# Optimization experiments

Measured on AMD Instinct MI355X. Metric: run time of the kernel, lower is better.

## Reference

```python
import jax, jax.numpy as jnp
import numpy as np

N_TOKEN = 267735
D_EMBED = 1024
D_PROJ = 1024
DIV_VAL = 4
CUTOFFS = [20000, 40000, 200000, N_TOKEN]   # cutoffs + [n_token]
ENDS = [0] + CUTOFFS                         # cutoff_ends
N_CLUSTERS = len(CUTOFFS) - 1                # 3
HEAD_SIZE = CUTOFFS[0] + N_CLUSTERS          # 20003
N = 1024                                     # len*bsz


def setup_inputs() -> dict:
    key = jax.random.key(0)
    ks = jax.random.split(key, 16)
    d_embs = [D_EMBED // DIV_VAL ** i for i in range(4)]  # 1024,256,64,16
    sizes = [HEAD_SIZE] + [ENDS[i + 1] - ENDS[i] for i in range(1, 4)]  # 20003,20000,160000,67735
    s = 0.02
    inp = {
        'hidden': jax.random.normal(ks[0], (N, D_PROJ), dtype=jnp.float32),
        'target': jax.random.randint(ks[1], (N,), 0, N_TOKEN, dtype=jnp.int32),
    }
    for i in range(4):
        inp[f'w{i}'] = jax.random.normal(ks[2 + 3 * i], (sizes[i], d_embs[i]), dtype=jnp.float32) * s
        inp[f'b{i}'] = jnp.zeros((sizes[i],), dtype=jnp.float32)
        inp[f'p{i}'] = jax.random.normal(ks[3 + 3 * i], (D_PROJ, d_embs[i]), dtype=jnp.float32) * s
    return inp


def _logit(h, w, b, p):
    # F.linear(hidden, proj.t()) -> h @ p ; F.linear(., weight, bias) -> @ w.T + b
    return (h @ p) @ w.T + b


def reference(hidden, target, w0, b0, p0, w1, b1, p1, w2, b2, p2, w3, b3, p3):
    head_lp = jax.nn.log_softmax(_logit(hidden, w0, b0, p0), axis=1)  # [N, HEAD_SIZE]
    tails = [(w1, b1, p1), (w2, b2, p2), (w3, b3, p3)]
    lps = []
    # shortlist cluster: gather target logprob directly from head
    t0 = jnp.clip(target, 0, CUTOFFS[0] - 1)
    lps.append(jnp.take_along_axis(head_lp, t0[:, None], axis=1)[:, 0])
    # tail clusters: small projected matmul + log_softmax + gather, combined with cluster logprob head_lp[:, -i]
    for i in range(1, 4):
        l, r = ENDS[i], ENDS[i + 1]
        ti = jnp.clip(target - l, 0, r - l - 1)
        tail_lp = jax.nn.log_softmax(_logit(hidden, *tails[i - 1]), axis=1)  # [N, r-l]
        lps.append(head_lp[:, -i] + jnp.take_along_axis(tail_lp, ti[:, None], axis=1)[:, 0])
    masks = [(target >= ENDS[i]) & (target < ENDS[i + 1]) for i in range(4)]
    logprob = jnp.select(masks, lps)
    return -logprob  # [N] per-token NLL, original order (keep_order=True)
```

## Files before the change

kernel.cpp:

```cpp
#include <hip/hip_runtime.h>
#include <hip/hip_bf16.h>
#include <math.h>

#define NTOK 1024
#define DPROJ 1024
#define PSTRIDE 1376
#define HEADS 20003
#define LOG2E 1.4426950408889634f
#define LN2   0.6931471805599453f
#define WSCALE (4.0f * LOG2E)
#define PSCALE 0.25f

#if __has_builtin(__builtin_amdgcn_exp2f)
#define EXP2(x) __builtin_amdgcn_exp2f(x)
#else
#define EXP2(x) exp2f(x)
#endif

#define MFMA8(a, b, c) __builtin_amdgcn_mfma_f32_16x16x32_fp8_fp8(a, b, c, 0, 0, 0)

typedef __attribute__((ext_vector_type(8))) short bf16x8;
typedef __attribute__((ext_vector_type(4))) float f32x4;
typedef long long i64;

__device__ __forceinline__ short f2bf(float f) {
    unsigned u = __float_as_uint(f);
    u += 0x7fffu + ((u >> 16) & 1u);
    return (short)(u >> 16);
}
__device__ __forceinline__ unsigned pk4fp8(float a, float b, float c, float d) {
    unsigned v = __builtin_amdgcn_cvt_pk_fp8_f32(a, b, 0, false);
    v = __builtin_amdgcn_cvt_pk_fp8_f32(c, d, v, true);
    return v;
}
__device__ __forceinline__ unsigned char fp8_1(float a) {
    return (unsigned char)(__builtin_amdgcn_cvt_pk_fp8_f32(a, a, 0, false) & 0xff);
}
__device__ __forceinline__ i64 wfrag(const float* wp) {
    float4 x = *(const float4*)(wp);
    float4 y = *(const float4*)(wp + 4);
    unsigned lo = pk4fp8(x.x * WSCALE, x.y * WSCALE, x.z * WSCALE, x.w * WSCALE);
    unsigned hi = pk4fp8(y.x * WSCALE, y.y * WSCALE, y.z * WSCALE, y.w * WSCALE);
    return (i64)(((unsigned long long)hi << 32) | lo);
}

#define NB0 157
#define NB1 79
#define NB2 625
#define NB3 265
#define NBTOT (NB0 + NB1 + NB2 + NB3)

#define EB0N 20096
#define EB1N 20224
#define EB2N 160000
#define EB3N 67840
#define EBTOT (EB0N + EB1N + EB2N + EB3N)

__global__ __launch_bounds__(256) void prep(const float* __restrict__ hidden,
                                            const float* __restrict__ p0,
                                            const float* __restrict__ p1,
                                            const float* __restrict__ p2,
                                            const float* __restrict__ p3,
                                            const float* __restrict__ b0,
                                            const float* __restrict__ b1,
                                            const float* __restrict__ b2,
                                            const float* __restrict__ b3,
                                            short* __restrict__ hbP,
                                            short* __restrict__ pTbP0,
                                            short* __restrict__ pTbP1,
                                            short* __restrict__ pTbP2,
                                            short* __restrict__ pTbP3,
                                            float* __restrict__ sums,
                                            unsigned char* __restrict__ pk3,
                                            float* __restrict__ eb0,
                                            float* __restrict__ eb1,
                                            float* __restrict__ eb2,
                                            float* __restrict__ eb3) {
    __shared__ float tile[64][65];
    int bid = blockIdx.x, tid = threadIdx.x;
    if (bid >= 418) {
        int g = (bid - 418) * 256 + tid;
        if (g < EB0N) {
            eb0[g] = (g < HEADS) ? exp2f(b0[g] * LOG2E) : 0.f;
        } else if (g < EB0N + EB1N) {
            int i = g - EB0N;
            eb1[i] = (i < 20000) ? exp2f(b1[i] * LOG2E) : 0.f;
        } else if (g < EB0N + EB1N + EB2N) {
            int i = g - EB0N - EB1N;
            eb2[i] = exp2f(b2[i] * LOG2E);
        } else if (g < EBTOT) {
            int i = g - EB0N - EB1N - EB2N;
            eb3[i] = (i < 67735) ? exp2f(b3[i] * LOG2E) : 0.f;
        }
        return;
    }
    if (bid == 416) {
        float4 z = {0.f, 0.f, 0.f, 0.f};
        #pragma unroll
        for (int i = 0; i < 4; ++i) *((float4*)sums + i * 256 + tid) = z;
        return;
    }
    if (bid == 417) {
        int4 z = {0, 0, 0, 0};
        #pragma unroll
        for (int i = 0; i < 8; ++i) *((int4*)pk3 + i * 256 + tid) = z;
        return;
    }
    if (bid < 64) {
        int tt = bid;
        #pragma unroll
        for (int q = 0; q < 8; ++q) {
            int fi = q * 256 + tid;
            int l = fi & 63;
            int row = tt * 16 + (l & 15);
            int kb = (fi >> 6) * 32 + (l >> 4) * 8;
            const float* hp = hidden + row * 1024 + kb;
            float4 x = *(const float4*)hp;
            float4 y = *(const float4*)(hp + 4);
            bf16x8 o;
            o[0]=f2bf(x.x); o[1]=f2bf(x.y); o[2]=f2bf(x.z); o[3]=f2bf(x.w);
            o[4]=f2bf(y.x); o[5]=f2bf(y.y); o[6]=f2bf(y.z); o[7]=f2bf(y.w);
            *(bf16x8*)(hbP + (size_t)tt * 16384 + fi * 8) = o;
        }
        return;
    }
    int lb = bid - 64;
    const float* p; short* dst; int d, kt, jb;
    if (lb < 256)      { p = p0; dst = pTbP0; d = 1024; kt = lb >> 4; jb = lb & 15; }
    else if (lb < 320) { lb -= 256; p = p1; dst = pTbP1; d = 256; kt = lb >> 2; jb = lb & 3; }
    else if (lb < 336) { lb -= 320; p = p2; dst = pTbP2; d = 64;  kt = lb; jb = 0; }
    else               { lb -= 336; p = p3; dst = pTbP3; d = 16;  kt = lb; jb = 0; }
    int k0 = kt * 64, j0 = jb * 64;
    int tx = tid & 63, ty = tid >> 6;
    #pragma unroll
    for (int rr = 0; rr < 16; ++rr) {
        int k = k0 + ty * 16 + rr;
        int j = j0 + tx;
        if (j < d) tile[ty * 16 + rr][tx] = p[k * d + j];
    }
    __syncthreads();
    int ch = tid >> 5;
    int jtl = ch >> 1, ksl = ch & 1;
    int jt = jb * 4 + jtl;
    if (jt * 16 < d) {
        #pragma unroll
        for (int li = 0; li < 2; ++li) {
            int l = (tid & 31) + li * 32;
            int jl = jtl * 16 + (l & 15);
            int kl = ksl * 32 + (l >> 4) * 8;
            bf16x8 o;
            #pragma unroll
            for (int e = 0; e < 8; ++e) o[e] = f2bf(tile[kl + e][jl]);
            *(bf16x8*)(dst + ((size_t)jt * 32 + kt * 2 + ksl) * 512 + l * 8) = o;
        }
    }
}

__global__ __launch_bounds__(256) void proj(const short* __restrict__ hbP,
                                            const short* __restrict__ pTbP0,
                                            const short* __restrict__ pTbP1,
                                            const short* __restrict__ pTbP2,
                                            const short* __restrict__ pTbP3,
                                            float* __restrict__ projf,
                                            unsigned char* __restrict__ pk0,
                                            unsigned char* __restrict__ pk1,
                                            unsigned char* __restrict__ pk2,
                                            unsigned char* __restrict__ pk3) {
    __shared__ float spackf[16][72];
    __shared__ unsigned char sp8[1024];
    int tt = blockIdx.x, jbG = blockIdx.y, tid = threadIdx.x;
    const short* pB; unsigned char* pkc; int d, KSp, coloff, jb;
    if (jbG < 16)      { pB = pTbP0; pkc = pk0; d = 1024; KSp = 32; coloff = 0;    jb = jbG; }
    else if (jbG < 20) { pB = pTbP1; pkc = pk1; d = 256;  KSp = 8;  coloff = 1024; jb = jbG - 16; }
    else if (jbG == 20){ pB = pTbP2; pkc = pk2; d = 64;   KSp = 2;  coloff = 1280; jb = 0; }
    else               { pB = pTbP3; pkc = pk3; d = 16;   KSp = 1;  coloff = 1344; jb = 0; }
    int w = tid >> 6, lane = tid & 63;
    int l16 = lane & 15, quad = lane >> 4;
    int jt = jb * 4 + w;
    if (jt * 16 < d) {
        const short* ap = hbP + ((size_t)tt * 32) * 512 + lane * 8;
        const short* bp = pB  + ((size_t)jt * 32) * 512 + lane * 8;
        f32x4 x0 = {0,0,0,0}, x1 = {0,0,0,0};
        #pragma unroll
        for (int ks = 0; ks < 16; ++ks) {
            bf16x8 a0 = *(const bf16x8*)(ap + ks * 512);
            bf16x8 b0 = *(const bf16x8*)(bp + ks * 512);
            bf16x8 a1 = *(const bf16x8*)(ap + (ks + 16) * 512);
            bf16x8 b1 = *(const bf16x8*)(bp + (ks + 16) * 512);
            x0 = __builtin_amdgcn_mfma_f32_16x16x32_bf16(a0, b0, x0, 0, 0, 0);
            x1 = __builtin_amdgcn_mfma_f32_16x16x32_bf16(a1, b1, x1, 0, 0, 0);
        }
        f32x4 acc = x0 + x1;
        int kk = w * 16 + l16;
        #pragma unroll
        for (int r = 0; r < 4; ++r) {
            int tok = quad * 4 + r;
            spackf[tok][kk] = acc[r];
            sp8[(kk >> 5) * 512 + ((kk & 31) >> 3) * 128 + tok * 8 + (kk & 7)] = fp8_1(acc[r] * PSCALE);
        }
    }
    __syncthreads();
    int j0g = jb * 64;
    int dcols = min(64, d - j0g);
    {
        int row = tid >> 4, cb = (tid & 15) * 4;
        if (cb < dcols) {
            float4 v = *(const float4*)&spackf[row][cb];
            *(float4*)&projf[(tt * 16 + row) * PSTRIDE + coloff + j0g + cb] = v;
        }
    }
    {
        int nbytes = 16 * dcols;
        if (tid * 4 < nbytes) {
            unsigned char* gdst = pkc + ((size_t)tt * KSp + (j0g >> 5)) * 512;
            *(unsigned*)(gdst + tid * 4) = *(const unsigned*)(sp8 + tid * 4);
        }
    }
}

__device__ __forceinline__ void stage16k(const unsigned char* g, unsigned char* l,
                                         int wave, int lane) {
    const unsigned char* gs = g + wave * 4096 + lane * 16;
    unsigned char* ls = l + wave * 4096;
    #pragma unroll
    for (int i = 0; i < 4; ++i)
        __builtin_amdgcn_global_load_lds(
            (const __attribute__((address_space(1))) unsigned*)(gs + i * 1024),
            (__attribute__((address_space(3))) unsigned*)(ls + i * 1024), 16, 0, 0);
}

__device__ __forceinline__ void lse_head(const float* __restrict__ w,
                                         const float* __restrict__ eb,
                                         const unsigned char* __restrict__ pk,
                                         float* __restrict__ part, int bid,
                                         unsigned char (*sbuf)[16384], float* bsum) {
    int tid = threadIdx.x;
    int wave = tid >> 6, lane = tid & 63;
    int quad = lane >> 4, l16 = lane & 15;
    int v0 = bid * 128 + wave * 32;

    for (int i = tid; i < NTOK; i += 256) bsum[i] = 0.f;

    i64 areg[2][32];
    float ee[2][4];
    #pragma unroll
    for (int vt = 0; vt < 2; ++vt) {
        int va = v0 + vt * 16 + l16;
        #pragma unroll
        for (int ks = 0; ks < 32; ++ks) {
            areg[vt][ks] = (va < HEADS) ? wfrag(w + (long)va * 1024 + ks * 32 + quad * 8) : 0;
        }
        #pragma unroll
        for (int r = 0; r < 4; ++r)
            ee[vt][r] = eb[v0 + vt * 16 + quad * 4 + r];
    }

    stage16k(pk, sbuf[0], wave, lane);
    __syncthreads();
    for (int tt = 0; tt < 64; ++tt) {
        if (tt < 63) stage16k(pk + (size_t)(tt + 1) * 16384, sbuf[(tt + 1) & 1], wave, lane);
        const unsigned char* sb = sbuf[tt & 1];
        f32x4 x0 = {0,0,0,0}, x1 = x0, x2 = x0, x3 = x0;
        __builtin_amdgcn_s_setprio(1);
        #pragma unroll
        for (int j = 0; j < 16; ++j) {
            i64 b0 = *(const i64*)(sb + j * 512 + lane * 8);
            i64 b1 = *(const i64*)(sb + (j + 16) * 512 + lane * 8);
            x0 = MFMA8(areg[0][j],      b0, x0);
            x1 = MFMA8(areg[0][j + 16], b1, x1);
            x2 = MFMA8(areg[1][j],      b0, x2);
            x3 = MFMA8(areg[1][j + 16], b1, x3);
        }
        __builtin_amdgcn_s_setprio(0);
        f32x4 a0 = x0 + x1, a1 = x2 + x3;
        float e0 = EXP2(a0[0]) * ee[0][0], e1 = EXP2(a0[1]) * ee[0][1];
        e0 += EXP2(a0[2]) * ee[0][2];  e1 += EXP2(a0[3]) * ee[0][3];
        e0 += EXP2(a1[0]) * ee[1][0];  e1 += EXP2(a1[1]) * ee[1][1];
        e0 += EXP2(a1[2]) * ee[1][2];  e1 += EXP2(a1[3]) * ee[1][3];
        float e = e0 + e1;
        e += __shfl_xor(e, 16, 64);
        e += __shfl_xor(e, 32, 64);
        if (lane < 16) atomicAdd(&bsum[tt * 16 + lane], e);
        __syncthreads();
    }
    *((float4*)part + tid) = *((const float4*)bsum + tid);
}

template <int KS, int VT>
__device__ __forceinline__ void lse_tail(const float* __restrict__ w,
                                         const float* __restrict__ eb,
                                         const unsigned char* __restrict__ pk,
                                         float* __restrict__ part,
                                         int V, int D, int bid, float* bsum) {
    int tid = threadIdx.x;
    int wave = tid >> 6, lane = tid & 63;
    int quad = lane >> 4, l16 = lane & 15;
    int v0 = bid * (64 * VT) + wave * (16 * VT);

    for (int i = tid; i < NTOK; i += 256) bsum[i] = 0.f;
    __syncthreads();

    i64 areg[VT][KS];
    float ee[VT][4];
    #pragma unroll
    for (int vt = 0; vt < VT; ++vt) {
        int va = v0 + vt * 16 + l16;
        #pragma unroll
        for (int ks = 0; ks < KS; ++ks) {
            int k = ks * 32 + quad * 8;
            areg[vt][ks] = (va < V && k < D) ? wfrag(w + (long)va * D + k) : 0;
        }
        #pragma unroll
        for (int r = 0; r < 4; ++r)
            ee[vt][r] = eb[v0 + vt * 16 + quad * 4 + r];
    }

    const i64* base = (const i64*)pk;
    i64 bn[KS];
    #pragma unroll
    for (int k = 0; k < KS; ++k) bn[k] = base[k * 64 + lane];
    for (int tt = 0; tt < 64; ++tt) {
        i64 bc[KS];
        #pragma unroll
        for (int k = 0; k < KS; ++k) bc[k] = bn[k];
        if (tt < 63) {
            const i64* nb = base + (size_t)(tt + 1) * KS * 64;
            #pragma unroll
            for (int k = 0; k < KS; ++k) bn[k] = nb[k * 64 + lane];
        }
        f32x4 accs[VT];
        __builtin_amdgcn_s_setprio(1);
        #pragma unroll
        for (int vt = 0; vt < VT; ++vt) {
            if constexpr (KS >= 4) {
                f32x4 y0 = {0,0,0,0}, y1 = {0,0,0,0};
                #pragma unroll
                for (int j = 0; j < KS / 2; ++j) {
                    y0 = MFMA8(areg[vt][j],          bc[j],          y0);
                    y1 = MFMA8(areg[vt][KS/2 + j],   bc[KS/2 + j],   y1);
                }
                accs[vt] = y0 + y1;
            } else if constexpr (KS == 2) {
                f32x4 y = {0,0,0,0};
                y = MFMA8(areg[vt][0], bc[0], y);
                y = MFMA8(areg[vt][1], bc[1], y);
                accs[vt] = y;
            } else {
                f32x4 y = {0,0,0,0};
                accs[vt] = MFMA8(areg[vt][0], bc[0], y);
            }
        }
        __builtin_amdgcn_s_setprio(0);
        float e0 = 0.f, e1 = 0.f;
        #pragma unroll
        for (int vt = 0; vt < VT; ++vt) {
            e0 += EXP2(accs[vt][0]) * ee[vt][0];
            e1 += EXP2(accs[vt][1]) * ee[vt][1];
            e0 += EXP2(accs[vt][2]) * ee[vt][2];
            e1 += EXP2(accs[vt][3]) * ee[vt][3];
        }
        float e = e0 + e1;
        e += __shfl_xor(e, 16, 64);
        e += __shfl_xor(e, 32, 64);
        if (lane < 16) atomicAdd(&bsum[tt * 16 + lane], e);
    }
    __syncthreads();
    *((float4*)part + tid) = *((const float4*)bsum + tid);
}

__global__ __launch_bounds__(256, 2) void lse_all(const float* __restrict__ w0, const float* __restrict__ eb0,
                                                  const float* __restrict__ w1, const float* __restrict__ eb1,
                                                  const float* __restrict__ w2, const float* __restrict__ eb2,
                                                  const float* __restrict__ w3, const float* __restrict__ eb3,
                                                  const unsigned char* __restrict__ pk0,
                                                  const unsigned char* __restrict__ pk1,
                                                  const unsigned char* __restrict__ pk2,
                                                  const unsigned char* __restrict__ pk3,
                                                  float* __restrict__ part) {
    __shared__ unsigned char sbuf[2][16384];
    __shared__ float bsum[NTOK];
    int bid = blockIdx.x;
    float* slab = part + (size_t)bid * NTOK;
    if (bid < NB0) {
        lse_head(w0, eb0, pk0, slab, bid, sbuf, bsum);
    } else if (bid < NB0 + NB1) {
        lse_tail<8, 4>(w1, eb1, pk1, slab, 20000,  256, bid - NB0, bsum);
    } else if (bid < NB0 + NB1 + NB2) {
        lse_tail<2, 4>(w2, eb2, pk2, slab, 160000, 64,  bid - NB0 - NB1, bsum);
    } else {
        lse_tail<1, 4>(w3, eb3, pk3, slab, 67735,  16,  bid - NB0 - NB1 - NB2, bsum);
    }
}

__global__ __launch_bounds__(256) void reduce_part(const float* __restrict__ part,
                                                   float* __restrict__ sums) {
    int bid = blockIdx.x;
    int c = bid >> 5, rem = bid & 31, q = rem >> 3, sl = rem & 7;
    const int off[4] = {0, NB0, NB0 + NB1, NB0 + NB1 + NB2};
    const int cnt[4] = {NB0, NB1, NB2, NB3};
    int tok = q * 256 + threadIdx.x;
    const float* p = part + (size_t)off[c] * NTOK + tok;
    int n = cnt[c];
    float s0 = 0.f, s1 = 0.f, s2 = 0.f, s3 = 0.f;
    int b = sl;
    for (; b + 24 < n; b += 32) {
        s0 += p[(size_t)b * NTOK];
        s1 += p[(size_t)(b + 8) * NTOK];
        s2 += p[(size_t)(b + 16) * NTOK];
        s3 += p[(size_t)(b + 24) * NTOK];
    }
    for (; b < n; b += 8) s0 += p[(size_t)b * NTOK];
    float s = (s0 + s1) + (s2 + s3);
    atomicAdd(&sums[c * NTOK + tok], s);
}

__global__ __launch_bounds__(256) void finalize(const int* __restrict__ target,
                                                const float* __restrict__ projf,
                                                const float* __restrict__ sums,
                                                const float* __restrict__ w0, const float* __restrict__ b0,
                                                const float* __restrict__ w1, const float* __restrict__ b1,
                                                const float* __restrict__ w2, const float* __restrict__ b2,
                                                const float* __restrict__ w3, const float* __restrict__ b3,
                                                float* __restrict__ out) {
    int wave = threadIdx.x >> 6, lane = threadIdx.x & 63;
    int row = blockIdx.x * 4 + wave;
    int t = target[row];
    int c = (t < 20000) ? 0 : (t < 40000) ? 1 : (t < 200000) ? 2 : 3;
    int col0 = (c == 0) ? t : (HEADS - c);
    const float* pr = projf + row * PSTRIDE;

    float s = 0.f;
    for (int k = lane; k < DPROJ; k += 64) s += pr[k] * w0[col0 * DPROJ + k];
    #pragma unroll
    for (int off = 32; off; off >>= 1) s += __shfl_xor(s, off, 64);
    float hl = s + b0[col0];
    float lse0 = __log2f(sums[row]) * LN2;

    float res;
    if (c == 0) {
        res = lse0 - hl;
    } else {
        const float* wc; const float* bc; int d, coloff, l;
        if (c == 1)      { wc = w1; bc = b1; d = 256; coloff = 1024; l = 20000; }
        else if (c == 2) { wc = w2; bc = b2; d = 64;  coloff = 1280; l = 40000; }
        else             { wc = w3; bc = b3; d = 16;  coloff = 1344; l = 200000; }
        int tc = t - l;
        float s2 = 0.f;
        for (int k = lane; k < d; k += 64) s2 += pr[coloff + k] * wc[tc * d + k];
        #pragma unroll
        for (int off = 32; off; off >>= 1) s2 += __shfl_xor(s2, off, 64);
        float tl = s2 + bc[tc];
        float lsec = __log2f(sums[c * NTOK + row]) * LN2;
        res = lse0 - hl + lsec - tl;
    }
    if (lane == 0) out[row] = res;
}


extern "C" void kernel_launch(void* const* d_in, const int* in_sizes, int n_in,
                              void* d_out, int out_size, void* d_ws, size_t ws_size,
                              hipStream_t stream) {
    const float* hidden = (const float*)d_in[0];
    const int*   target = (const int*)d_in[1];
    const float* w0 = (const float*)d_in[2];
    const float* b0 = (const float*)d_in[3];
    const float* p0 = (const float*)d_in[4];
    const float* w1 = (const float*)d_in[5];
    const float* b1 = (const float*)d_in[6];
    const float* p1 = (const float*)d_in[7];
    const float* w2 = (const float*)d_in[8];
    const float* b2 = (const float*)d_in[9];
    const float* p2 = (const float*)d_in[10];
    const float* w3 = (const float*)d_in[11];
    const float* b3 = (const float*)d_in[12];
    const float* p3 = (const float*)d_in[13];

    short* base = (short*)d_ws;
    short* hbP   = base;
    short* pTbP0 = base + 1048576;
    short* pTbP1 = base + 2097152;
    short* pTbP2 = base + 2359296;
    short* pTbP3 = base + 2424832;
    float* projf = (float*)((char*)d_ws + 4882432);
    unsigned char* pk0 = (unsigned char*)d_ws + 10518528;
    unsigned char* pk1 = pk0 + 1048576;
    unsigned char* pk2 = pk1 + 262144;
    unsigned char* pk3 = pk2 + 65536;
    float* sums  = (float*)((char*)d_ws + 11927552);
    float* part  = (float*)((char*)d_ws + 11943936);
    float* eb0   = (float*)((char*)d_ws + 16556032);
    float* eb1   = (float*)((char*)d_ws + 16636416);
    float* eb2   = (float*)((char*)d_ws + 16717312);
    float* eb3   = (float*)((char*)d_ws + 17357312);

    prep<<<1466, 256, 0, stream>>>(hidden, p0, p1, p2, p3, b0, b1, b2, b3,
                                   hbP, pTbP0, pTbP1, pTbP2, pTbP3, sums, pk3,
                                   eb0, eb1, eb2, eb3);
    proj<<<dim3(64, 22), 256, 0, stream>>>(hbP, pTbP0, pTbP1, pTbP2, pTbP3,
                                           projf, pk0, pk1, pk2, pk3);
    lse_all<<<NBTOT, 256, 0, stream>>>(w0, eb0, w1, eb1, w2, eb2, w3, eb3,
                                       pk0, pk1, pk2, pk3, part);
    reduce_part<<<128, 256, 0, stream>>>(part, sums);
    finalize<<<256, 256, 0, stream>>>(target, projf, sums,
                                      w0, b0, w1, b1, w2, b2, w3, b3, (float*)d_out);
}
```

Measured before the change: 323.6 us.

## Split head and tail LSE into separate kernels with token-halved head blocks

Splits the fused lse_all kernel into a head kernel and a tails kernel. The head kernel now uses twice as many blocks, each covering half the tokens, so the 157-block head work spreads across more CUs, and each half-block writes into its half of a shared slab. The tail kernel drops the 32KB LDS staging buffer, raises launch bounds to 4 blocks per CU and changes the vocab-tile template parameters (fewer blocks for clusters 2 and 3). Exp-bias padding and the workspace offsets are adjusted to match. The trade-off is that each head block now reloads its full weight fragments for only half the token work, which doubles the head weight reads. It also adds a launch, and the two kernels on the same stream run back to back rather than overlapping.

```diff
diff --git a/kernel.cpp b/kernel.cpp
--- a/kernel.cpp
+++ b/kernel.cpp
@@ -45,15 +45,17 @@
 }
 
 #define NB0 157
-#define NB1 79
-#define NB2 625
-#define NB3 265
-#define NBTOT (NB0 + NB1 + NB2 + NB3)
+#define NB0G 314
+#define NB1T 157
+#define NB2T 313
+#define NB3T 133
+#define NBT (NB1T + NB2T + NB3T)
+#define NSLAB (NB0 + NBT)
 
 #define EB0N 20096
-#define EB1N 20224
-#define EB2N 160000
-#define EB3N 67840
+#define EB1N 20096
+#define EB2N 160256
+#define EB3N 68096
 #define EBTOT (EB0N + EB1N + EB2N + EB3N)
 
 __global__ __launch_bounds__(256) void prep(const float* __restrict__ hidden,
@@ -87,7 +89,7 @@
             eb1[i] = (i < 20000) ? exp2f(b1[i] * LOG2E) : 0.f;
         } else if (g < EB0N + EB1N + EB2N) {
             int i = g - EB0N - EB1N;
-            eb2[i] = exp2f(b2[i] * LOG2E);
+            eb2[i] = (i < 160000) ? exp2f(b2[i] * LOG2E) : 0.f;
         } else if (g < EBTOT) {
             int i = g - EB0N - EB1N - EB2N;
             eb3[i] = (i < 67735) ? exp2f(b3[i] * LOG2E) : 0.f;
@@ -229,17 +231,20 @@
             (__attribute__((address_space(3))) unsigned*)(ls + i * 1024), 16, 0, 0);
 }
 
-__device__ __forceinline__ void lse_head(const float* __restrict__ w,
-                                         const float* __restrict__ eb,
-                                         const unsigned char* __restrict__ pk,
-                                         float* __restrict__ part, int bid,
-                                         unsigned char (*sbuf)[16384], float* bsum) {
+__global__ __launch_bounds__(256, 1) void lse_head_k(const float* __restrict__ w,
+                                                     const float* __restrict__ eb,
+                                                     const unsigned char* __restrict__ pk,
+                                                     float* __restrict__ part) {
+    __shared__ unsigned char sbuf[2][16384];
+    __shared__ float bsum[512];
+    int bid = blockIdx.x;
+    int bh = bid >> 1, th = bid & 1;
     int tid = threadIdx.x;
     int wave = tid >> 6, lane = tid & 63;
     int quad = lane >> 4, l16 = lane & 15;
-    int v0 = bid * 128 + wave * 32;
-
-    for (int i = tid; i < NTOK; i += 256) bsum[i] = 0.f;
+    int v0 = bh * 128 + wave * 32;
+
+    for (int i = tid; i < 512; i += 256) bsum[i] = 0.f;
 
     i64 areg[2][32];
     float ee[2][4];
@@ -247,19 +252,19 @@
     for (int vt = 0; vt < 2; ++vt) {
         int va = v0 + vt * 16 + l16;
         #pragma unroll
-        for (int ks = 0; ks < 32; ++ks) {
+        for (int ks = 0; ks < 32; ++ks)
             areg[vt][ks] = (va < HEADS) ? wfrag(w + (long)va * 1024 + ks * 32 + quad * 8) : 0;
-        }
         #pragma unroll
         for (int r = 0; r < 4; ++r)
             ee[vt][r] = eb[v0 + vt * 16 + quad * 4 + r];
     }
 
-    stage16k(pk, sbuf[0], wave, lane);
+    const unsigned char* pkt = pk + (size_t)th * 32 * 16384;
+    stage16k(pkt, sbuf[0], wave, lane);
     __syncthreads();
-    for (int tt = 0; tt < 64; ++tt) {
-        if (tt < 63) stage16k(pk + (size_t)(tt + 1) * 16384, sbuf[(tt + 1) & 1], wave, lane);
-        const unsigned char* sb = sbuf[tt & 1];
+    for (int t = 0; t < 32; ++t) {
+        if (t < 31) stage16k(pkt + (size_t)(t + 1) * 16384, sbuf[(t + 1) & 1], wave, lane);
+        const unsigned char* sb = sbuf[t & 1];
         f32x4 x0 = {0,0,0,0}, x1 = x0, x2 = x0, x3 = x0;
         __builtin_amdgcn_s_setprio(1);
         #pragma unroll
@@ -280,10 +285,11 @@
         float e = e0 + e1;
         e += __shfl_xor(e, 16, 64);
         e += __shfl_xor(e, 32, 64);
-        if (lane < 16) atomicAdd(&bsum[tt * 16 + lane], e);
+        if (lane < 16) atomicAdd(&bsum[t * 16 + lane], e);
         __syncthreads();
     }
-    *((float4*)part + tid) = *((const float4*)bsum + tid);
+    if (tid < 128)
+        ((float4*)(part + (size_t)bh * NTOK + th * 512))[tid] = ((const float4*)bsum)[tid];
 }
 
 template <int KS, int VT>
@@ -368,27 +374,22 @@
     *((float4*)part + tid) = *((const float4*)bsum + tid);
 }
 
-__global__ __launch_bounds__(256, 2) void lse_all(const float* __restrict__ w0, const float* __restrict__ eb0,
-                                                  const float* __restrict__ w1, const float* __restrict__ eb1,
-                                                  const float* __restrict__ w2, const float* __restrict__ eb2,
-                                                  const float* __restrict__ w3, const float* __restrict__ eb3,
-                                                  const unsigned char* __restrict__ pk0,
-                                                  const unsigned char* __restrict__ pk1,
-                                                  const unsigned char* __restrict__ pk2,
-                                                  const unsigned char* __restrict__ pk3,
-                                                  float* __restrict__ part) {
-    __shared__ unsigned char sbuf[2][16384];
+__global__ __launch_bounds__(256, 4) void lse_tails(const float* __restrict__ w1, const float* __restrict__ eb1,
+                                                    const float* __restrict__ w2, const float* __restrict__ eb2,
+                                                    const float* __restrict__ w3, const float* __restrict__ eb3,
+                                                    const unsigned char* __restrict__ pk1,
+                                                    const unsigned char* __restrict__ pk2,
+                                                    const unsigned char* __restrict__ pk3,
+                                                    float* __restrict__ part) {
     __shared__ float bsum[NTOK];
     int bid = blockIdx.x;
-    float* slab = part + (size_t)bid * NTOK;
-    if (bid < NB0) {
-        lse_head(w0, eb0, pk0, slab, bid, sbuf, bsum);
-    } else if (bid < NB0 + NB1) {
-        lse_tail<8, 4>(w1, eb1, pk1, slab, 20000,  256, bid - NB0, bsum);
-    } else if (bid < NB0 + NB1 + NB2) {
-        lse_tail<2, 4>(w2, eb2, pk2, slab, 160000, 64,  bid - NB0 - NB1, bsum);
+    float* slab = part + (size_t)(NB0 + bid) * NTOK;
+    if (bid < NB1T) {
+        lse_tail<8, 2>(w1, eb1, pk1, slab, 20000,  256, bid, bsum);
+    } else if (bid < NB1T + NB2T) {
+        lse_tail<2, 8>(w2, eb2, pk2, slab, 160000, 64,  bid - NB1T, bsum);
     } else {
-        lse_tail<1, 4>(w3, eb3, pk3, slab, 67735,  16,  bid - NB0 - NB1 - NB2, bsum);
+        lse_tail<1, 8>(w3, eb3, pk3, slab, 67735,  16,  bid - NB1T - NB2T, bsum);
     }
 }
 
@@ -396,8 +397,8 @@
                                                    float* __restrict__ sums) {
     int bid = blockIdx.x;
     int c = bid >> 5, rem = bid & 31, q = rem >> 3, sl = rem & 7;
-    const int off[4] = {0, NB0, NB0 + NB1, NB0 + NB1 + NB2};
-    const int cnt[4] = {NB0, NB1, NB2, NB3};
+    const int off[4] = {0, NB0, NB0 + NB1T, NB0 + NB1T + NB2T};
+    const int cnt[4] = {NB0, NB1T, NB2T, NB3T};
     int tok = q * 256 + threadIdx.x;
     const float* p = part + (size_t)off[c] * NTOK + tok;
     int n = cnt[c];
@@ -488,18 +489,19 @@
     unsigned char* pk3 = pk2 + 65536;
     float* sums  = (float*)((char*)d_ws + 11927552);
     float* part  = (float*)((char*)d_ws + 11943936);
-    float* eb0   = (float*)((char*)d_ws + 16556032);
-    float* eb1   = (float*)((char*)d_ws + 16636416);
-    float* eb2   = (float*)((char*)d_ws + 16717312);
-    float* eb3   = (float*)((char*)d_ws + 17357312);
-
-    prep<<<1466, 256, 0, stream>>>(hidden, p0, p1, p2, p3, b0, b1, b2, b3,
+    float* eb0   = (float*)((char*)d_ws + 15056896);
+    float* eb1   = (float*)((char*)d_ws + 15137280);
+    float* eb2   = (float*)((char*)d_ws + 15217664);
+    float* eb3   = (float*)((char*)d_ws + 15858688);
+
+    prep<<<1467, 256, 0, stream>>>(hidden, p0, p1, p2, p3, b0, b1, b2, b3,
                                    hbP, pTbP0, pTbP1, pTbP2, pTbP3, sums, pk3,
                                    eb0, eb1, eb2, eb3);
     proj<<<dim3(64, 22), 256, 0, stream>>>(hbP, pTbP0, pTbP1, pTbP2, pTbP3,
                                            projf, pk0, pk1, pk2, pk3);
-    lse_all<<<NBTOT, 256, 0, stream>>>(w0, eb0, w1, eb1, w2, eb2, w3, eb3,
-                                       pk0, pk1, pk2, pk3, part);
+    lse_head_k<<<NB0G, 256, 0, stream>>>(w0, eb0, pk0, part);
+    lse_tails<<<NBT, 256, 0, stream>>>(w1, eb1, w2, eb2, w3, eb3,
+                                       pk1, pk2, pk3, part);
     reduce_part<<<128, 256, 0, stream>>>(part, sums);
     finalize<<<256, 256, 0, stream>>>(target, projf, sums,
                                       w0, b0, w1, b1, w2, b2, w3, b3, (float*)d_out);
```

After: 342.5 us. 5.8% more time.

## Interleave fp8 projected fragments for 16-byte loads and rebalance vocab blocks per cluster

Applied to the files above, without the earlier changes.

Reorders the fp8 packed projection layout so pairs of K-slices are adjacent, letting the LSE kernels fetch two MFMA B-fragments with one 16-byte load. It also rebalances the work per block: head blocks now cover 64 vocab rows instead of 128 (halving the register-held weight fragments), the tail1 blocks use fewer vocab tiles and the tail2/tail3 blocks use more, and the padded bias-exp buffers are resized to match. The intent is fewer load instructions, less register pressure in the head, and better load balance across the grid, at the cost of more partial slabs to reduce and more redundant streaming of the projected activations.

```diff
diff --git a/kernel.cpp b/kernel.cpp
--- a/kernel.cpp
+++ b/kernel.cpp
@@ -22,6 +22,7 @@
 typedef __attribute__((ext_vector_type(8))) short bf16x8;
 typedef __attribute__((ext_vector_type(4))) float f32x4;
 typedef long long i64;
+typedef __attribute__((ext_vector_type(2))) long long i64x2;
 
 __device__ __forceinline__ short f2bf(float f) {
     unsigned u = __float_as_uint(f);
@@ -44,16 +45,16 @@
     return (i64)(((unsigned long long)hi << 32) | lo);
 }
 
-#define NB0 157
-#define NB1 79
-#define NB2 625
-#define NB3 265
-#define NBTOT (NB0 + NB1 + NB2 + NB3)
+#define NB0H 313
+#define NB1T 157
+#define NB2T 313
+#define NB3T 133
+#define NSLAB (NB0H + NB1T + NB2T + NB3T)
 
 #define EB0N 20096
-#define EB1N 20224
-#define EB2N 160000
-#define EB3N 67840
+#define EB1N 20096
+#define EB2N 160256
+#define EB3N 68096
 #define EBTOT (EB0N + EB1N + EB2N + EB3N)
 
 __global__ __launch_bounds__(256) void prep(const float* __restrict__ hidden,
@@ -87,7 +88,7 @@
             eb1[i] = (i < 20000) ? exp2f(b1[i] * LOG2E) : 0.f;
         } else if (g < EB0N + EB1N + EB2N) {
             int i = g - EB0N - EB1N;
-            eb2[i] = exp2f(b2[i] * LOG2E);
+            eb2[i] = (i < 160000) ? exp2f(b2[i] * LOG2E) : 0.f;
         } else if (g < EBTOT) {
             int i = g - EB0N - EB1N - EB2N;
             eb3[i] = (i < 67735) ? exp2f(b3[i] * LOG2E) : 0.f;
@@ -196,7 +197,10 @@
         for (int r = 0; r < 4; ++r) {
             int tok = quad * 4 + r;
             spackf[tok][kk] = acc[r];
-            sp8[(kk >> 5) * 512 + ((kk & 31) >> 3) * 128 + tok * 8 + (kk & 7)] = fp8_1(acc[r] * PSCALE);
+            int idx;
+            if (d > 16) idx = ((kk & 31) >> 3) * 256 + tok * 16 + (kk >> 5) * 8 + (kk & 7);
+            else        idx = ((kk & 31) >> 3) * 128 + tok * 8 + (kk & 7);
+            sp8[idx] = fp8_1(acc[r] * PSCALE);
         }
     }
     __syncthreads();
@@ -237,46 +241,37 @@
     int tid = threadIdx.x;
     int wave = tid >> 6, lane = tid & 63;
     int quad = lane >> 4, l16 = lane & 15;
-    int v0 = bid * 128 + wave * 32;
+    int v0 = bid * 64 + wave * 16;
 
     for (int i = tid; i < NTOK; i += 256) bsum[i] = 0.f;
 
-    i64 areg[2][32];
-    float ee[2][4];
+    i64 areg[32];
+    float ee[4];
+    int va = v0 + l16;
     #pragma unroll
-    for (int vt = 0; vt < 2; ++vt) {
-        int va = v0 + vt * 16 + l16;
-        #pragma unroll
-        for (int ks = 0; ks < 32; ++ks) {
-            areg[vt][ks] = (va < HEADS) ? wfrag(w + (long)va * 1024 + ks * 32 + quad * 8) : 0;
-        }
-        #pragma unroll
-        for (int r = 0; r < 4; ++r)
-            ee[vt][r] = eb[v0 + vt * 16 + quad * 4 + r];
-    }
+    for (int ks = 0; ks < 32; ++ks)
+        areg[ks] = (va < HEADS) ? wfrag(w + (long)va * 1024 + ks * 32 + quad * 8) : 0;
+    #pragma unroll
+    for (int r = 0; r < 4; ++r)
+        ee[r] = eb[v0 + quad * 4 + r];
 
     stage16k(pk, sbuf[0], wave, lane);
     __syncthreads();
     for (int tt = 0; tt < 64; ++tt) {
         if (tt < 63) stage16k(pk + (size_t)(tt + 1) * 16384, sbuf[(tt + 1) & 1], wave, lane);
         const unsigned char* sb = sbuf[tt & 1];
-        f32x4 x0 = {0,0,0,0}, x1 = x0, x2 = x0, x3 = x0;
+        f32x4 x0 = {0,0,0,0}, x1 = x0;
         __builtin_amdgcn_s_setprio(1);
         #pragma unroll
-        for (int j = 0; j < 16; ++j) {
-            i64 b0 = *(const i64*)(sb + j * 512 + lane * 8);
-            i64 b1 = *(const i64*)(sb + (j + 16) * 512 + lane * 8);
-            x0 = MFMA8(areg[0][j],      b0, x0);
-            x1 = MFMA8(areg[0][j + 16], b1, x1);
-            x2 = MFMA8(areg[1][j],      b0, x2);
-            x3 = MFMA8(areg[1][j + 16], b1, x3);
+        for (int p = 0; p < 16; ++p) {
+            i64x2 b2 = *(const i64x2*)(sb + p * 1024 + lane * 16);
+            x0 = MFMA8(areg[2 * p],     b2[0], x0);
+            x1 = MFMA8(areg[2 * p + 1], b2[1], x1);
         }
         __builtin_amdgcn_s_setprio(0);
-        f32x4 a0 = x0 + x1, a1 = x2 + x3;
-        float e0 = EXP2(a0[0]) * ee[0][0], e1 = EXP2(a0[1]) * ee[0][1];
-        e0 += EXP2(a0[2]) * ee[0][2];  e1 += EXP2(a0[3]) * ee[0][3];
-        e0 += EXP2(a1[0]) * ee[1][0];  e1 += EXP2(a1[1]) * ee[1][1];
-        e0 += EXP2(a1[2]) * ee[1][2];  e1 += EXP2(a1[3]) * ee[1][3];
+        f32x4 a = x0 + x1;
+        float e0 = EXP2(a[0]) * ee[0] + EXP2(a[2]) * ee[2];
+        float e1 = EXP2(a[1]) * ee[1] + EXP2(a[3]) * ee[3];
         float e = e0 + e1;
         e += __shfl_xor(e, 16, 64);
         e += __shfl_xor(e, 32, 64);
@@ -315,54 +310,63 @@
             ee[vt][r] = eb[v0 + vt * 16 + quad * 4 + r];
     }
 
-    const i64* base = (const i64*)pk;
-    i64 bn[KS];
-    #pragma unroll
-    for (int k = 0; k < KS; ++k) bn[k] = base[k * 64 + lane];
-    for (int tt = 0; tt < 64; ++tt) {
-        i64 bc[KS];
-        #pragma unroll
-        for (int k = 0; k < KS; ++k) bc[k] = bn[k];
-        if (tt < 63) {
-            const i64* nb = base + (size_t)(tt + 1) * KS * 64;
+    if constexpr (KS >= 2) {
+        constexpr int KSP = KS / 2;
+        i64x2 bn[KSP], bc[KSP];
+        #pragma unroll
+        for (int p = 0; p < KSP; ++p)
+            bn[p] = *(const i64x2*)(pk + p * 1024 + lane * 16);
+        for (int tt = 0; tt < 64; ++tt) {
             #pragma unroll
-            for (int k = 0; k < KS; ++k) bn[k] = nb[k * 64 + lane];
-        }
-        f32x4 accs[VT];
-        __builtin_amdgcn_s_setprio(1);
-        #pragma unroll
-        for (int vt = 0; vt < VT; ++vt) {
-            if constexpr (KS >= 4) {
+            for (int p = 0; p < KSP; ++p) bc[p] = bn[p];
+            if (tt < 63) {
+                const unsigned char* nb = pk + (size_t)(tt + 1) * (KS * 512);
+                #pragma unroll
+                for (int p = 0; p < KSP; ++p)
+                    bn[p] = *(const i64x2*)(nb + p * 1024 + lane * 16);
+            }
+            float e0 = 0.f, e1 = 0.f;
+            #pragma unroll
+            for (int vt = 0; vt < VT; ++vt) {
                 f32x4 y0 = {0,0,0,0}, y1 = {0,0,0,0};
+                __builtin_amdgcn_s_setprio(1);
                 #pragma unroll
-                for (int j = 0; j < KS / 2; ++j) {
-                    y0 = MFMA8(areg[vt][j],          bc[j],          y0);
-                    y1 = MFMA8(areg[vt][KS/2 + j],   bc[KS/2 + j],   y1);
+                for (int p = 0; p < KSP; ++p) {
+                    y0 = MFMA8(areg[vt][2 * p],     bc[p][0], y0);
+                    y1 = MFMA8(areg[vt][2 * p + 1], bc[p][1], y1);
                 }
-                accs[vt] = y0 + y1;
-            } else if constexpr (KS == 2) {
-                f32x4 y = {0,0,0,0};
-                y = MFMA8(areg[vt][0], bc[0], y);
-                y = MFMA8(areg[vt][1], bc[1], y);
-                accs[vt] = y;
-            } else {
-                f32x4 y = {0,0,0,0};
-                accs[vt] = MFMA8(areg[vt][0], bc[0], y);
+                __builtin_amdgcn_s_setprio(0);
+                f32x4 a = y0 + y1;
+                e0 += EXP2(a[0]) * ee[vt][0];
+                e1 += EXP2(a[1]) * ee[vt][1];
+                e0 += EXP2(a[2]) * ee[vt][2];
+                e1 += EXP2(a[3]) * ee[vt][3];
             }
-        }
-        __builtin_amdgcn_s_setprio(0);
-        float e0 = 0.f, e1 = 0.f;
-        #pragma unroll
-        for (int vt = 0; vt < VT; ++vt) {
-            e0 += EXP2(accs[vt][0]) * ee[vt][0];
-            e1 += EXP2(accs[vt][1]) * ee[vt][1];
-            e0 += EXP2(accs[vt][2]) * ee[vt][2];
-            e1 += EXP2(accs[vt][3]) * ee[vt][3];
-        }
-        float e = e0 + e1;
-        e += __shfl_xor(e, 16, 64);
-        e += __shfl_xor(e, 32, 64);
-        if (lane < 16) atomicAdd(&bsum[tt * 16 + lane], e);
+            float e = e0 + e1;
+            e += __shfl_xor(e, 16, 64);
+            e += __shfl_xor(e, 32, 64);
+            if (lane < 16) atomicAdd(&bsum[tt * 16 + lane], e);
+        }
+    } else {
+        i64 bn = *(const i64*)(pk + lane * 8);
+        for (int tt = 0; tt < 64; ++tt) {
+            i64 bc = bn;
+            if (tt < 63) bn = *(const i64*)(pk + (size_t)(tt + 1) * 512 + lane * 8);
+            float e0 = 0.f, e1 = 0.f;
+            #pragma unroll
+            for (int vt = 0; vt < VT; ++vt) {
+                f32x4 y0 = {0,0,0,0};
+                f32x4 a = MFMA8(areg[vt][0], bc, y0);
+                e0 += EXP2(a[0]) * ee[vt][0];
+                e1 += EXP2(a[1]) * ee[vt][1];
+                e0 += EXP2(a[2]) * ee[vt][2];
+                e1 += EXP2(a[3]) * ee[vt][3];
+            }
+            float e = e0 + e1;
+            e += __shfl_xor(e, 16, 64);
+            e += __shfl_xor(e, 32, 64);
+            if (lane < 16) atomicAdd(&bsum[tt * 16 + lane], e);
+        }
     }
     __syncthreads();
     *((float4*)part + tid) = *((const float4*)bsum + tid);
@@ -381,14 +385,14 @@
     __shared__ float bsum[NTOK];
     int bid = blockIdx.x;
     float* slab = part + (size_t)bid * NTOK;
-    if (bid < NB0) {
+    if (bid < NB0H) {
         lse_head(w0, eb0, pk0, slab, bid, sbuf, bsum);
-    } else if (bid < NB0 + NB1) {
-        lse_tail<8, 4>(w1, eb1, pk1, slab, 20000,  256, bid - NB0, bsum);
-    } else if (bid < NB0 + NB1 + NB2) {
-        lse_tail<2, 4>(w2, eb2, pk2, slab, 160000, 64,  bid - NB0 - NB1, bsum);
+    } else if (bid < NB0H + NB1T) {
+        lse_tail<8, 2>(w1, eb1, pk1, slab, 20000,  256, bid - NB0H, bsum);
+    } else if (bid < NB0H + NB1T + NB2T) {
+        lse_tail<2, 8>(w2, eb2, pk2, slab, 160000, 64,  bid - NB0H - NB1T, bsum);
     } else {
-        lse_tail<1, 4>(w3, eb3, pk3, slab, 67735,  16,  bid - NB0 - NB1 - NB2, bsum);
+        lse_tail<1, 8>(w3, eb3, pk3, slab, 67735,  16,  bid - NB0H - NB1T - NB2T, bsum);
     }
 }
 
@@ -396,8 +400,8 @@
                                                    float* __restrict__ sums) {
     int bid = blockIdx.x;
     int c = bid >> 5, rem = bid & 31, q = rem >> 3, sl = rem & 7;
-    const int off[4] = {0, NB0, NB0 + NB1, NB0 + NB1 + NB2};
-    const int cnt[4] = {NB0, NB1, NB2, NB3};
+    const int off[4] = {0, NB0H, NB0H + NB1T, NB0H + NB1T + NB2T};
+    const int cnt[4] = {NB0H, NB1T, NB2T, NB3T};
     int tok = q * 256 + threadIdx.x;
     const float* p = part + (size_t)off[c] * NTOK + tok;
     int n = cnt[c];
@@ -488,17 +492,17 @@
     unsigned char* pk3 = pk2 + 65536;
     float* sums  = (float*)((char*)d_ws + 11927552);
     float* part  = (float*)((char*)d_ws + 11943936);
-    float* eb0   = (float*)((char*)d_ws + 16556032);
-    float* eb1   = (float*)((char*)d_ws + 16636416);
-    float* eb2   = (float*)((char*)d_ws + 16717312);
-    float* eb3   = (float*)((char*)d_ws + 17357312);
-
-    prep<<<1466, 256, 0, stream>>>(hidden, p0, p1, p2, p3, b0, b1, b2, b3,
+    float* eb0   = (float*)((char*)d_ws + 15695872);
+    float* eb1   = (float*)((char*)d_ws + 15776256);
+    float* eb2   = (float*)((char*)d_ws + 15856640);
+    float* eb3   = (float*)((char*)d_ws + 16497664);
+
+    prep<<<1467, 256, 0, stream>>>(hidden, p0, p1, p2, p3, b0, b1, b2, b3,
                                    hbP, pTbP0, pTbP1, pTbP2, pTbP3, sums, pk3,
                                    eb0, eb1, eb2, eb3);
     proj<<<dim3(64, 22), 256, 0, stream>>>(hbP, pTbP0, pTbP1, pTbP2, pTbP3,
                                            projf, pk0, pk1, pk2, pk3);
-    lse_all<<<NBTOT, 256, 0, stream>>>(w0, eb0, w1, eb1, w2, eb2, w3, eb3,
+    lse_all<<<NSLAB, 256, 0, stream>>>(w0, eb0, w1, eb1, w2, eb2, w3, eb3,
                                        pk0, pk1, pk2, pk3, part);
     reduce_part<<<128, 256, 0, stream>>>(part, sums);
     finalize<<<256, 256, 0, stream>>>(target, projf, sums,
```

New measurement: 310.6 us. 1.04x faster.
